# Optimization experiments

Measured on AMD Instinct MI355X. Metric: run time of the kernel, lower is better.

## Reference

```python
import jax, jax.numpy as jnp
import numpy as np

D_MODEL = 2048
N_HEADS = 16
D_HEAD = D_MODEL // N_HEADS  # 128
RANK = 32


def _orthogonal(key, rows, cols, dtype=jnp.float32):
    # mimic torch orthogonal init via QR
    a = jax.random.normal(key, (max(rows, cols), min(rows, cols)), dtype=jnp.float32)
    q, r = jnp.linalg.qr(a)
    q = q * jnp.sign(jnp.diagonal(r))
    if rows < cols:
        q = q.T
    return q.astype(dtype)


def setup_inputs() -> dict:
    key = jax.random.key(0)
    ks = jax.random.split(key, 8)
    B, T = 2, 2048
    x = jax.random.normal(ks[0], (B, T, D_MODEL), dtype=jnp.float32)
    s = 1.0 / np.sqrt(D_MODEL)
    Wq = jax.random.uniform(ks[1], (D_MODEL, D_MODEL), minval=-s, maxval=s, dtype=jnp.float32)
    Wk = jax.random.uniform(ks[2], (D_MODEL, D_MODEL), minval=-s, maxval=s, dtype=jnp.float32)
    Wv = jax.random.uniform(ks[3], (D_MODEL, D_MODEL), minval=-s, maxval=s, dtype=jnp.float32)
    Wo = jax.random.uniform(ks[4], (D_MODEL, D_MODEL), minval=-s, maxval=s, dtype=jnp.float32)
    # vein projector: project d_head -> rank, reconstruct rank -> d_head (orthogonal init)
    Wdown = _orthogonal(ks[5], D_HEAD, RANK)   # [d_head, r]
    Wup = _orthogonal(ks[6], RANK, D_HEAD)     # [r, d_head]
    return {"x": x, "Wq": Wq, "Wk": Wk, "Wv": Wv, "Wo": Wo, "Wdown": Wdown, "Wup": Wup}


def reference(x, Wq, Wk, Wv, Wo, Wdown, Wup):
    B, T, D = x.shape
    H, dh, r = N_HEADS, D_HEAD, RANK
    scale = 1.0 / np.sqrt(r)

    def heads(y):  # [B,T,D] -> [B,H,T,dh]
        return y.reshape(B, T, H, dh).transpose(0, 2, 1, 3)

    q = heads(x @ Wq.T)
    k = heads(x @ Wk.T)
    v = heads(x @ Wv.T)

    # project into vein (rank) space: [B,H,T,r]
    q_r = jnp.einsum('bhtd,dr->bhtr', q, Wdown)
    k_r = jnp.einsum('bhtd,dr->bhtr', k, Wdown)
    v_r = jnp.einsum('bhtd,dr->bhtr', v, Wdown)

    scores = jnp.einsum('bhqr,bhkr->bhqk', q_r, k_r) * scale  # [B,H,T,T]
    attn = jax.nn.softmax(scores, axis=-1)
    y_r = jnp.einsum('bhqk,bhkr->bhqr', attn, v_r)            # [B,H,T,r]
    y = jnp.einsum('bhtr,rd->bhtd', y_r, Wup)                  # reconstruct [B,H,T,dh]
    y = y.transpose(0, 2, 1, 3).reshape(B, T, D)
    out = y @ Wo.T
    return out
```

## Files before the change

### kernel.cpp

```cpp
#include <hip/hip_runtime.h>
#include <cstdint>
#include <cstddef>

typedef __bf16 bf16;
typedef __attribute__((ext_vector_type(8))) __bf16 bf16x8;
typedef __attribute__((ext_vector_type(4))) __bf16 bf16x4;
typedef __attribute__((ext_vector_type(2))) __bf16 bf16x2;
typedef __attribute__((ext_vector_type(4))) float f32x4;
typedef unsigned int u32;

#define D_MODEL 2048
#define QSCALE      0.17677669529663687f
#define QSCALE_L2E  (0.17677669529663687f * 1.4426950408889634f)

__device__ inline void async_load16(const void* gp, void* lp) {
  __builtin_amdgcn_global_load_lds(
      (const __attribute__((address_space(1))) u32*)gp,
      (__attribute__((address_space(3))) u32*)lp, 16, 0, 0);
}

__device__ inline float fast_exp2(float x) {
#if __has_builtin(__builtin_amdgcn_exp2f)
  return __builtin_amdgcn_exp2f(x);
#else
  return __expf(x * 0.6931471805599453f);
#endif
}

__global__ __launch_bounds__(256) void prep_k(
    const float* __restrict__ x,  const float* __restrict__ Wq,
    const float* __restrict__ Wk, const float* __restrict__ Wv,
    const float* __restrict__ Wo, const float* __restrict__ Wdown,
    const float* __restrict__ Wup,
    bf16* __restrict__ xb, bf16* __restrict__ EffT,
    bf16* __restrict__ WoEffT) {
  __shared__ __align__(16) char smem_[40960];
  const int bid = blockIdx.x;
  const int t = threadIdx.x;

  if (bid < 768) {
    const int mh = bid % 48;
    const int dblk = bid / 48;
    const float* W = (mh < 16) ? Wq : ((mh < 32) ? Wk : Wv);
    const int hrow = (mh & 15) * 128;
    const int d = dblk * 128 + (t & 127);
    const int rh = (t >> 7) * 16;
    const int rhs = __builtin_amdgcn_readfirstlane(rh);
    const float* wdn = Wdown + rhs;
    float acc[16];
#pragma unroll
    for (int j = 0; j < 16; ++j) acc[j] = 0.f;
    for (int kb = 0; kb < 16; ++kb) {
      float wv[8];
#pragma unroll
      for (int u = 0; u < 8; ++u)
        wv[u] = W[(size_t)(hrow + kb * 8 + u) * D_MODEL + d];
#pragma unroll
      for (int u = 0; u < 8; ++u) {
#pragma unroll
        for (int j = 0; j < 16; ++j)
          acc[j] += wv[u] * wdn[(kb * 8 + u) * 32 + j];
      }
    }
    bf16* outp = EffT + (size_t)(mh * 32 + rh) * D_MODEL + d;
#pragma unroll
    for (int j = 0; j < 16; ++j) outp[(size_t)j * D_MODEL] = (bf16)acc[j];
    return;
  }

  if (bid >= 1024) {
    const int tid = (bid - 1024) * 256 + t;
    float4 v[8];
#pragma unroll
    for (int p = 0; p < 4; ++p) {
      const int i = (tid + p * 262144) * 8;
      v[2 * p]     = *(const float4*)(x + i);
      v[2 * p + 1] = *(const float4*)(x + i + 4);
    }
#pragma unroll
    for (int p = 0; p < 4; ++p) {
      const int i = (tid + p * 262144) * 8;
      bf16x8 o;
      o[0] = (bf16)v[2*p].x;   o[1] = (bf16)v[2*p].y;
      o[2] = (bf16)v[2*p].z;   o[3] = (bf16)v[2*p].w;
      o[4] = (bf16)v[2*p+1].x; o[5] = (bf16)v[2*p+1].y;
      o[6] = (bf16)v[2*p+1].z; o[7] = (bf16)v[2*p+1].w;
      *(bf16x8*)(xb + i) = o;
    }
    return;
  }

  bf16* As_ = (bf16*)smem_;
  bf16* Bs_ = (bf16*)(smem_ + 32768);
  const int rel = bid - 768;
  const int d0 = (rel & 15) * 128, h = rel >> 4;
  const int wave = t >> 6, lane = t & 63;
  const int quad = lane >> 4, lc = lane & 15;
#pragma unroll
  for (int a = 0; a < 8; ++a) {
    int cc = a * 256 + t;
    int row = cc >> 4, c = cc & 15;
    const float* src = Wo + (size_t)(d0 + row) * 2048 + h * 128 + c * 8;
    float4 f0 = ((const float4*)src)[0], f1 = ((const float4*)src)[1];
    bf16x8 v;
    v[0] = (bf16)f0.x; v[1] = (bf16)f0.y; v[2] = (bf16)f0.z; v[3] = (bf16)f0.w;
    v[4] = (bf16)f1.x; v[5] = (bf16)f1.y; v[6] = (bf16)f1.z; v[7] = (bf16)f1.w;
    *(bf16x8*)(As_ + row * 128 + ((c ^ (row & 15)) * 8)) = v;
  }
  {
    int row = t >> 3;
    int c0 = (t & 7) * 2;
    const float* src = Wup + row * 128 + c0 * 8;
    float4 f0 = ((const float4*)src)[0], f1 = ((const float4*)src)[1];
    float4 f2 = ((const float4*)src)[2], f3 = ((const float4*)src)[3];
    bf16x8 b0, b1;
    b0[0] = (bf16)f0.x; b0[1] = (bf16)f0.y; b0[2] = (bf16)f0.z; b0[3] = (bf16)f0.w;
    b0[4] = (bf16)f1.x; b0[5] = (bf16)f1.y; b0[6] = (bf16)f1.z; b0[7] = (bf16)f1.w;
    b1[0] = (bf16)f2.x; b1[1] = (bf16)f2.y; b1[2] = (bf16)f2.z; b1[3] = (bf16)f2.w;
    b1[4] = (bf16)f3.x; b1[5] = (bf16)f3.y; b1[6] = (bf16)f3.z; b1[7] = (bf16)f3.w;
    *(bf16x8*)(Bs_ + row * 128 + ((c0 ^ (row & 15)) * 8)) = b0;
    *(bf16x8*)(Bs_ + row * 128 + (((c0 + 1) ^ (row & 15)) * 8)) = b1;
  }
  __syncthreads();
  f32x4 acc[2][2] = {};
  const int wm = wave * 32;
#pragma unroll
  for (int kc = 0; kc < 4; ++kc) {
    bf16x8 af[2], bfr[2];
#pragma unroll
    for (int mi = 0; mi < 2; ++mi) {
      int m = wm + mi * 16 + lc;
      af[mi] = *(const bf16x8*)(As_ + m * 128 + (((kc * 4 + quad) ^ (m & 15)) * 8));
    }
#pragma unroll
    for (int ni = 0; ni < 2; ++ni) {
      int n = ni * 16 + lc;
      bfr[ni] = *(const bf16x8*)(Bs_ + n * 128 + (((kc * 4 + quad) ^ (n & 15)) * 8));
    }
#pragma unroll
    for (int mi = 0; mi < 2; ++mi)
#pragma unroll
      for (int ni = 0; ni < 2; ++ni)
        acc[mi][ni] = __builtin_amdgcn_mfma_f32_16x16x32_bf16(
            af[mi], bfr[ni], acc[mi][ni], 0, 0, 0);
  }
#pragma unroll
  for (int mi = 0; mi < 2; ++mi)
#pragma unroll
    for (int ni = 0; ni < 2; ++ni)
#pragma unroll
      for (int reg = 0; reg < 4; ++reg)
        WoEffT[(size_t)(d0 + wm + mi * 16 + quad * 4 + reg) * 512 + h * 32 +
               ni * 16 + lc] = (bf16)acc[mi][ni][reg];
}

template <int EPI, int BM>
__global__ __launch_bounds__(256, (BM == 64 ? 3 : 2)) void gemm_bt_k(
    const bf16* __restrict__ A, const bf16* __restrict__ Bt,
    void* __restrict__ Cv, int M, int N, int K) {
  constexpr int MI = BM / 32;
  constexpr int AR = BM / 4;
  __shared__ __align__(16) bf16 As[2][BM * 64];
  __shared__ __align__(16) bf16 Bs[2][128 * 64];
  const int t = threadIdx.x, wave = t >> 6, lane = t & 63;
  const int quad = lane >> 4, lc = lane & 15;
  const size_t m0 = (size_t)blockIdx.x * BM;
  const size_t n0 = (size_t)blockIdx.y * 128;
  const int wm = (wave >> 1) * (MI * 16), wn = (wave & 1) * 64;
  const int sr = lane >> 3, ss = lane & 7;
  const bf16* Aga[MI]; const bf16* Bga[4]; int LoffA[MI], LoffB[4];
#pragma unroll
  for (int a = 0; a < MI; ++a) {
    int row = wave * AR + a * 8 + sr;
    Aga[a] = A + (m0 + row) * (size_t)K + (ss ^ (row & 7)) * 8;
    LoffA[a] = (wave * AR + a * 8) * 64;
  }
#pragma unroll
  for (int a = 0; a < 4; ++a) {
    int row = wave * 32 + a * 8 + sr;
    Bga[a] = Bt + (n0 + row) * (size_t)K + (ss ^ (row & 7)) * 8;
    LoffB[a] = (wave * 32 + a * 8) * 64;
  }
  f32x4 acc[MI][4] = {};
  const int NIT = K >> 6;
#pragma unroll
  for (int a = 0; a < MI; ++a) async_load16(Aga[a], &As[0][LoffA[a]]);
#pragma unroll
  for (int a = 0; a < 4; ++a) async_load16(Bga[a], &Bs[0][LoffB[a]]);
  __syncthreads();
  for (int it = 0; it < NIT; ++it) {
    const int cur = it & 1;
    if (it + 1 < NIT) {
      const int k0 = (it + 1) * 64;
#pragma unroll
      for (int a = 0; a < MI; ++a) async_load16(Aga[a] + k0, &As[1 - cur][LoffA[a]]);
#pragma unroll
      for (int a = 0; a < 4; ++a) async_load16(Bga[a] + k0, &Bs[1 - cur][LoffB[a]]);
    }
    const bf16* Asb = As[cur];
    const bf16* Bsb = Bs[cur];
#pragma unroll
    for (int kc = 0; kc < 2; ++kc) {
      bf16x8 af[MI], bfr[4];
#pragma unroll
      for (int mi = 0; mi < MI; ++mi) {
        int m = wm + mi * 16 + lc;
        af[mi] = *(const bf16x8*)(Asb + m * 64 + (((kc * 4 + quad) ^ (m & 7)) * 8));
      }
#pragma unroll
      for (int ni = 0; ni < 4; ++ni) {
        int n = wn + ni * 16 + lc;
        bfr[ni] = *(const bf16x8*)(Bsb + n * 64 + (((kc * 4 + quad) ^ (n & 7)) * 8));
      }
#pragma unroll
      for (int mi = 0; mi < MI; ++mi)
#pragma unroll
        for (int ni = 0; ni < 4; ++ni)
          acc[mi][ni] = __builtin_amdgcn_mfma_f32_16x16x32_bf16(
              af[mi], bfr[ni], acc[mi][ni], 0, 0, 0);
    }
    __syncthreads();
  }

  if (EPI == 0) {
    float* C = (float*)Cv;
#pragma unroll
    for (int mi = 0; mi < MI; ++mi)
#pragma unroll
      for (int ni = 0; ni < 4; ++ni) {
        size_t row = m0 + wm + mi * 16 + quad * 4;
        size_t col = n0 + wn + ni * 16 + lc;
#pragma unroll
        for (int reg = 0; reg < 4; ++reg)
          C[(row + reg) * (size_t)N + col] = acc[mi][ni][reg];
      }
  } else {
    bf16* C = (bf16*)Cv;
#pragma unroll
    for (int mi = 0; mi < MI; ++mi)
#pragma unroll
      for (int ni = 0; ni < 4; ++ni) {
        int n = (int)n0 + wn + ni * 16 + lc;
        int mat = n >> 9, hh = (n >> 5) & 15, r = n & 31;
        float sc = (mat == 0) ? QSCALE_L2E : 1.0f;
        int trow = (int)m0 + wm + mi * 16 + quad * 4;
        int b = trow >> 11, tl = trow & 2047;
        if (mat == 2) {
          int tile = tl >> 7, kin = tl & 127;
          size_t off = ((size_t)(b * 16 + hh) * 3 + 2) * 65536 +
                       (size_t)tile * 4096 + r * 128 +
                       (((kin >> 3) ^ (r & 15)) << 3) + (kin & 7);
          bf16x4 pk;
#pragma unroll
          for (int reg = 0; reg < 4; ++reg) pk[reg] = (bf16)acc[mi][ni][reg];
          *(bf16x4*)(C + off) = pk;
        } else {
#pragma unroll
          for (int reg = 0; reg < 4; ++reg) {
            size_t off = (((size_t)(b * 16 + hh) * 3 + mat) * 2048 + tl + reg) * 32 + r;
            C[off] = (bf16)(acc[mi][ni][reg] * sc);
          }
        }
      }
  }
}

__global__ __launch_bounds__(256, 4) void attn_k(const bf16* __restrict__ QKVr,
                                                 float* __restrict__ Op,
                                                 float* __restrict__ Sums) {
  const int bh = blockIdx.x, qb = blockIdx.y, kvh = blockIdx.z;
  const size_t base = (size_t)bh * 3 * 65536;
  const bf16* Q   = QKVr + base;
  const bf16* Kr  = Q + 65536 + (size_t)kvh * 1024 * 32;
  const bf16* Vrb = Q + 131072 + (size_t)kvh * 8 * 4096;
  __shared__ __align__(16) bf16 Ks[2][128 * 32];
  __shared__ __align__(16) bf16 Vt[2][32 * 128];
  __shared__ __align__(16) bf16 Ps[4 * 32 * 32];
  const int t = threadIdx.x, wave = t >> 6, lane = t & 63;
  const int quad = lane >> 4, lc = lane & 15;
  const int qbase = qb * 128 + wave * 32;
  const bf16x8 qf0 = *(const bf16x8*)(Q + (size_t)(qbase + lc) * 32 + quad * 8);
  const bf16x8 qf1 = *(const bf16x8*)(Q + (size_t)(qbase + 16 + lc) * 32 + quad * 8);
  f32x4 o00 = {}, o01 = {}, o10 = {}, o11 = {};
  f32x4 os0 = {}, os1 = {};
  bf16x8 ones;
#pragma unroll
  for (int j = 0; j < 8; ++j) ones[j] = (bf16)1.0f;
  const int krow = wave * 16 + (lane >> 2);
  const bf16* Kg = Kr + (size_t)krow * 32 + ((lane & 3) ^ ((krow >> 1) & 3)) * 8;
  bf16* pw = Ps + wave * 32 * 32;
  const int psw = (lc & 3) ^ (lc >> 2);

  async_load16(Kg, &Ks[0][wave * 16 * 32]);
  async_load16(Kg + (size_t)64 * 32, &Ks[0][(64 + wave * 16) * 32]);
  async_load16(Vrb + (wave * 2) * 512 + lane * 8, &Vt[0][(wave * 2) * 512]);
  async_load16(Vrb + (wave * 2 + 1) * 512 + lane * 8, &Vt[0][(wave * 2 + 1) * 512]);
  __syncthreads();

  for (int it = 0; it < 8; ++it) {
    const int kt = it * 128, cur = it & 1;
    if (it < 7) {
      async_load16(Kg + (size_t)(kt + 128) * 32, &Ks[1 - cur][wave * 16 * 32]);
      async_load16(Kg + (size_t)(kt + 192) * 32, &Ks[1 - cur][(64 + wave * 16) * 32]);
      const bf16* vg = Vrb + (size_t)(it + 1) * 4096;
      async_load16(vg + (wave * 2) * 512 + lane * 8, &Vt[1 - cur][(wave * 2) * 512]);
      async_load16(vg + (wave * 2 + 1) * 512 + lane * 8, &Vt[1 - cur][(wave * 2 + 1) * 512]);
    }
    const bf16* ksb = Ks[cur];
    const bf16* vtb = Vt[cur];
#pragma unroll
    for (int qtr = 0; qtr < 4; ++qtr) {
#pragma unroll
      for (int nii = 0; nii < 2; ++nii) {
        int ni = qtr * 2 + nii;
        int n = ni * 16 + lc;
        bf16x8 kf = *(const bf16x8*)(ksb + n * 32 + ((quad ^ ((n >> 1) & 3)) * 8));
        f32x4 z = {0.f, 0.f, 0.f, 0.f};
        f32x4 s0 = __builtin_amdgcn_mfma_f32_16x16x32_bf16(kf, qf0, z, 0, 0, 0);
        f32x4 s1 = __builtin_amdgcn_mfma_f32_16x16x32_bf16(kf, qf1, z, 0, 0, 0);
        bf16x4 p0, p1;
#pragma unroll
        for (int reg = 0; reg < 4; ++reg) {
          p0[reg] = (bf16)fast_exp2(s0[reg]);
          p1[reg] = (bf16)fast_exp2(s1[reg]);
        }
        int off = (((2 * nii + (quad >> 1)) ^ psw) * 8) + (quad & 1) * 4;
        *(bf16x4*)(pw + lc * 32 + off) = p0;
        *(bf16x4*)(pw + (16 + lc) * 32 + off) = p1;
      }
      int co = (quad ^ psw) * 8;
      bf16x8 pf0 = *(const bf16x8*)(pw + lc * 32 + co);
      bf16x8 pf1 = *(const bf16x8*)(pw + (16 + lc) * 32 + co);
      int vo = ((qtr * 4 + quad) ^ lc) * 8;
      bf16x8 v0 = *(const bf16x8*)(vtb + lc * 128 + vo);
      bf16x8 v1 = *(const bf16x8*)(vtb + (16 + lc) * 128 + vo);
      o00 = __builtin_amdgcn_mfma_f32_16x16x32_bf16(pf0, v0, o00, 0, 0, 0);
      o01 = __builtin_amdgcn_mfma_f32_16x16x32_bf16(pf0, v1, o01, 0, 0, 0);
      o10 = __builtin_amdgcn_mfma_f32_16x16x32_bf16(pf1, v0, o10, 0, 0, 0);
      o11 = __builtin_amdgcn_mfma_f32_16x16x32_bf16(pf1, v1, o11, 0, 0, 0);
      os0 = __builtin_amdgcn_mfma_f32_16x16x32_bf16(pf0, ones, os0, 0, 0, 0);
      os1 = __builtin_amdgcn_mfma_f32_16x16x32_bf16(pf1, ones, os1, 0, 0, 0);
    }
    __syncthreads();
  }
  const int b = bh >> 4, h = bh & 15;
  float* op = Op + (size_t)kvh * 4096 * 512;
#pragma unroll
  for (int reg = 0; reg < 4; ++reg) {
    size_t r0 = (size_t)b * 2048 + qbase + quad * 4 + reg;
    size_t r1 = r0 + 16;
    op[r0 * 512 + h * 32 + lc]      = o00[reg];
    op[r0 * 512 + h * 32 + 16 + lc] = o01[reg];
    op[r1 * 512 + h * 32 + lc]      = o10[reg];
    op[r1 * 512 + h * 32 + 16 + lc] = o11[reg];
  }
  if (lc == 0) {
    float* sp = Sums + (size_t)kvh * 65536 + (size_t)bh * 2048 + qbase;
#pragma unroll
    for (int reg = 0; reg < 4; ++reg) {
      sp[quad * 4 + reg]      = os0[reg];
      sp[16 + quad * 4 + reg] = os1[reg];
    }
  }
}

__global__ __launch_bounds__(256) void comb_k(const float* __restrict__ Op,
                                              const float* __restrict__ Sums,
                                              bf16* __restrict__ Yr) {
  const int idx = blockIdx.x * 256 + threadIdx.x;
  const int row = idx >> 6;
  const int c8 = (idx & 63) * 8;
  const int b = row >> 11, tl = row & 2047;
  const int h = c8 >> 5;
  const size_t si = (size_t)(b * 16 + h) * 2048 + tl;
  const float inv = 1.0f / (Sums[si] + Sums[65536 + si]);
  const float4* p0 = (const float4*)(Op + (size_t)row * 512 + c8);
  const float4* p1 = (const float4*)(Op + 4096 * 512 + (size_t)row * 512 + c8);
  float4 a0 = p0[0], a1 = p0[1];
  float4 b0 = p1[0], b1 = p1[1];
  bf16x8 o;
  o[0] = (bf16)((a0.x + b0.x) * inv); o[1] = (bf16)((a0.y + b0.y) * inv);
  o[2] = (bf16)((a0.z + b0.z) * inv); o[3] = (bf16)((a0.w + b0.w) * inv);
  o[4] = (bf16)((a1.x + b1.x) * inv); o[5] = (bf16)((a1.y + b1.y) * inv);
  o[6] = (bf16)((a1.z + b1.z) * inv); o[7] = (bf16)((a1.w + b1.w) * inv);
  *(bf16x8*)(Yr + (size_t)row * 512 + c8) = o;
}

extern "C" void kernel_launch(void* const* d_in, const int* in_sizes, int n_in,
                              void* d_out, int out_size, void* d_ws, size_t ws_size,
                              hipStream_t stream) {
  const float* x     = (const float*)d_in[0];
  const float* Wq    = (const float*)d_in[1];
  const float* Wk    = (const float*)d_in[2];
  const float* Wv    = (const float*)d_in[3];
  const float* Wo    = (const float*)d_in[4];
  const float* Wdown = (const float*)d_in[5];
  const float* Wup   = (const float*)d_in[6];
  float* out = (float*)d_out;

  char* ws = (char*)d_ws;
  bf16*  EffT   = (bf16*)(ws);
  float* Sums   = (float*)(ws);
  bf16*  WoEffT = (bf16*)(ws + 6291456);
  bf16*  QKVr   = (bf16*)(ws + 8388608);
  bf16*  Yrb    = (bf16*)(ws + 20971520);
  bf16*  xb     = (bf16*)(ws + 25165824);
  float* Opart  = (float*)(ws + 25165824);

  prep_k<<<dim3(2048), dim3(256), 0, stream>>>(x, Wq, Wk, Wv, Wo, Wdown, Wup,
                                               xb, EffT, WoEffT);
  gemm_bt_k<1, 64><<<dim3(64, 12), dim3(256), 0, stream>>>(xb, EffT, QKVr,
                                                           4096, 1536, 2048);
  attn_k<<<dim3(32, 16, 2), dim3(256), 0, stream>>>(QKVr, Opart, Sums);
  comb_k<<<dim3(1024), dim3(256), 0, stream>>>(Opart, Sums, Yrb);
  gemm_bt_k<0, 128><<<dim3(32, 16), dim3(256), 0, stream>>>(Yrb, WoEffT, out,
                                                            4096, 2048, 512);
}
```

Measured before the change: 224.4 us.

## Fuse fp32-to-bf16 conversion of x into QKV projection GEMM A-tile loads

The separate pass that converted x to bf16 inside prep_k is removed. The QKV GEMM now reads fp32 x directly, converts it in registers and writes swizzled bf16 tiles to shared memory, overlapping the next tile's global loads with the MFMA work. This removes one full write and read of the bf16 activation copy. The Wo-effective prep blocks are also re-split into smaller 64-row tiles so the prep grid shrinks, and the templated GEMM is split into two specialised kernels. The trade-off is that the A path moves from asynchronous direct-to-LDS loads to register-staged loads, which raises register pressure and doubles the bytes read for A inside the GEMM.

```diff
diff --git a/kernel.cpp b/kernel.cpp
--- a/kernel.cpp
+++ b/kernel.cpp
@@ -27,14 +27,19 @@
 #endif
 }
 
+__device__ inline bf16x8 cvt8(float4 a, float4 b) {
+  bf16x8 o;
+  o[0] = (bf16)a.x; o[1] = (bf16)a.y; o[2] = (bf16)a.z; o[3] = (bf16)a.w;
+  o[4] = (bf16)b.x; o[5] = (bf16)b.y; o[6] = (bf16)b.z; o[7] = (bf16)b.w;
+  return o;
+}
+
 __global__ __launch_bounds__(256) void prep_k(
-    const float* __restrict__ x,  const float* __restrict__ Wq,
-    const float* __restrict__ Wk, const float* __restrict__ Wv,
-    const float* __restrict__ Wo, const float* __restrict__ Wdown,
-    const float* __restrict__ Wup,
-    bf16* __restrict__ xb, bf16* __restrict__ EffT,
-    bf16* __restrict__ WoEffT) {
-  __shared__ __align__(16) char smem_[40960];
+    const float* __restrict__ Wq, const float* __restrict__ Wk,
+    const float* __restrict__ Wv, const float* __restrict__ Wo,
+    const float* __restrict__ Wdown, const float* __restrict__ Wup,
+    bf16* __restrict__ EffT, bf16* __restrict__ WoEffT) {
+  __shared__ __align__(16) char smem_[24576];
   const int bid = blockIdx.x;
   const int t = threadIdx.x;
 
@@ -68,44 +73,19 @@
     return;
   }
 
-  if (bid >= 1024) {
-    const int tid = (bid - 1024) * 256 + t;
-    float4 v[8];
-#pragma unroll
-    for (int p = 0; p < 4; ++p) {
-      const int i = (tid + p * 262144) * 8;
-      v[2 * p]     = *(const float4*)(x + i);
-      v[2 * p + 1] = *(const float4*)(x + i + 4);
-    }
-#pragma unroll
-    for (int p = 0; p < 4; ++p) {
-      const int i = (tid + p * 262144) * 8;
-      bf16x8 o;
-      o[0] = (bf16)v[2*p].x;   o[1] = (bf16)v[2*p].y;
-      o[2] = (bf16)v[2*p].z;   o[3] = (bf16)v[2*p].w;
-      o[4] = (bf16)v[2*p+1].x; o[5] = (bf16)v[2*p+1].y;
-      o[6] = (bf16)v[2*p+1].z; o[7] = (bf16)v[2*p+1].w;
-      *(bf16x8*)(xb + i) = o;
-    }
-    return;
-  }
-
   bf16* As_ = (bf16*)smem_;
-  bf16* Bs_ = (bf16*)(smem_ + 32768);
+  bf16* Bs_ = (bf16*)(smem_ + 16384);
   const int rel = bid - 768;
-  const int d0 = (rel & 15) * 128, h = rel >> 4;
+  const int d0 = (rel & 31) * 64, h = rel >> 5;
   const int wave = t >> 6, lane = t & 63;
   const int quad = lane >> 4, lc = lane & 15;
 #pragma unroll
-  for (int a = 0; a < 8; ++a) {
+  for (int a = 0; a < 4; ++a) {
     int cc = a * 256 + t;
     int row = cc >> 4, c = cc & 15;
     const float* src = Wo + (size_t)(d0 + row) * 2048 + h * 128 + c * 8;
     float4 f0 = ((const float4*)src)[0], f1 = ((const float4*)src)[1];
-    bf16x8 v;
-    v[0] = (bf16)f0.x; v[1] = (bf16)f0.y; v[2] = (bf16)f0.z; v[3] = (bf16)f0.w;
-    v[4] = (bf16)f1.x; v[5] = (bf16)f1.y; v[6] = (bf16)f1.z; v[7] = (bf16)f1.w;
-    *(bf16x8*)(As_ + row * 128 + ((c ^ (row & 15)) * 8)) = v;
+    *(bf16x8*)(As_ + row * 128 + ((c ^ (row & 15)) * 8)) = cvt8(f0, f1);
   }
   {
     int row = t >> 3;
@@ -113,97 +93,183 @@
     const float* src = Wup + row * 128 + c0 * 8;
     float4 f0 = ((const float4*)src)[0], f1 = ((const float4*)src)[1];
     float4 f2 = ((const float4*)src)[2], f3 = ((const float4*)src)[3];
-    bf16x8 b0, b1;
-    b0[0] = (bf16)f0.x; b0[1] = (bf16)f0.y; b0[2] = (bf16)f0.z; b0[3] = (bf16)f0.w;
-    b0[4] = (bf16)f1.x; b0[5] = (bf16)f1.y; b0[6] = (bf16)f1.z; b0[7] = (bf16)f1.w;
-    b1[0] = (bf16)f2.x; b1[1] = (bf16)f2.y; b1[2] = (bf16)f2.z; b1[3] = (bf16)f2.w;
-    b1[4] = (bf16)f3.x; b1[5] = (bf16)f3.y; b1[6] = (bf16)f3.z; b1[7] = (bf16)f3.w;
-    *(bf16x8*)(Bs_ + row * 128 + ((c0 ^ (row & 15)) * 8)) = b0;
-    *(bf16x8*)(Bs_ + row * 128 + (((c0 + 1) ^ (row & 15)) * 8)) = b1;
+    *(bf16x8*)(Bs_ + row * 128 + ((c0 ^ (row & 15)) * 8)) = cvt8(f0, f1);
+    *(bf16x8*)(Bs_ + row * 128 + (((c0 + 1) ^ (row & 15)) * 8)) = cvt8(f2, f3);
   }
   __syncthreads();
-  f32x4 acc[2][2] = {};
-  const int wm = wave * 32;
+  f32x4 acc[2] = {};
+  const int wm = wave * 16;
 #pragma unroll
   for (int kc = 0; kc < 4; ++kc) {
-    bf16x8 af[2], bfr[2];
-#pragma unroll
-    for (int mi = 0; mi < 2; ++mi) {
-      int m = wm + mi * 16 + lc;
-      af[mi] = *(const bf16x8*)(As_ + m * 128 + (((kc * 4 + quad) ^ (m & 15)) * 8));
-    }
+    int m = wm + lc;
+    bf16x8 af = *(const bf16x8*)(As_ + m * 128 + (((kc * 4 + quad) ^ (m & 15)) * 8));
 #pragma unroll
     for (int ni = 0; ni < 2; ++ni) {
       int n = ni * 16 + lc;
-      bfr[ni] = *(const bf16x8*)(Bs_ + n * 128 + (((kc * 4 + quad) ^ (n & 15)) * 8));
-    }
-#pragma unroll
-    for (int mi = 0; mi < 2; ++mi)
-#pragma unroll
-      for (int ni = 0; ni < 2; ++ni)
-        acc[mi][ni] = __builtin_amdgcn_mfma_f32_16x16x32_bf16(
-            af[mi], bfr[ni], acc[mi][ni], 0, 0, 0);
-  }
-#pragma unroll
-  for (int mi = 0; mi < 2; ++mi)
-#pragma unroll
-    for (int ni = 0; ni < 2; ++ni)
-#pragma unroll
-      for (int reg = 0; reg < 4; ++reg)
-        WoEffT[(size_t)(d0 + wm + mi * 16 + quad * 4 + reg) * 512 + h * 32 +
-               ni * 16 + lc] = (bf16)acc[mi][ni][reg];
-}
-
-template <int EPI, int BM>
-__global__ __launch_bounds__(256, (BM == 64 ? 3 : 2)) void gemm_bt_k(
-    const bf16* __restrict__ A, const bf16* __restrict__ Bt,
-    void* __restrict__ Cv, int M, int N, int K) {
-  constexpr int MI = BM / 32;
-  constexpr int AR = BM / 4;
-  __shared__ __align__(16) bf16 As[2][BM * 64];
+      bf16x8 bfr = *(const bf16x8*)(Bs_ + n * 128 + (((kc * 4 + quad) ^ (n & 15)) * 8));
+      acc[ni] = __builtin_amdgcn_mfma_f32_16x16x32_bf16(af, bfr, acc[ni], 0, 0, 0);
+    }
+  }
+#pragma unroll
+  for (int ni = 0; ni < 2; ++ni)
+#pragma unroll
+    for (int reg = 0; reg < 4; ++reg)
+      WoEffT[(size_t)(d0 + wm + quad * 4 + reg) * 512 + h * 32 +
+             ni * 16 + lc] = (bf16)acc[ni][reg];
+}
+
+__global__ __launch_bounds__(256, 3) void gemm1_k(
+    const float* __restrict__ Ax, const bf16* __restrict__ Bt,
+    bf16* __restrict__ C, int M, int N, int K) {
+  __shared__ __align__(16) bf16 As[2][64 * 64];
   __shared__ __align__(16) bf16 Bs[2][128 * 64];
   const int t = threadIdx.x, wave = t >> 6, lane = t & 63;
   const int quad = lane >> 4, lc = lane & 15;
-  const size_t m0 = (size_t)blockIdx.x * BM;
+  const size_t m0 = (size_t)blockIdx.x * 64;
   const size_t n0 = (size_t)blockIdx.y * 128;
-  const int wm = (wave >> 1) * (MI * 16), wn = (wave & 1) * 64;
+  const int wm = (wave >> 1) * 32, wn = (wave & 1) * 64;
   const int sr = lane >> 3, ss = lane & 7;
-  const bf16* Aga[MI]; const bf16* Bga[4]; int LoffA[MI], LoffB[4];
-#pragma unroll
-  for (int a = 0; a < MI; ++a) {
-    int row = wave * AR + a * 8 + sr;
-    Aga[a] = A + (m0 + row) * (size_t)K + (ss ^ (row & 7)) * 8;
-    LoffA[a] = (wave * AR + a * 8) * 64;
-  }
+  const int arow = t >> 2;
+  const int ac0 = (t & 3) * 2;
+  const float* Aga = Ax + (m0 + arow) * (size_t)K + ac0 * 8;
+  bf16* aw0;
+  bf16* aw1;
+  {
+    int s0 = (ac0 ^ (arow & 7)) * 8, s1 = ((ac0 + 1) ^ (arow & 7)) * 8;
+    aw0 = (bf16*)As + arow * 64 + s0;
+    aw1 = (bf16*)As + arow * 64 + s1;
+  }
+  const bf16* Bga[4]; int LoffB[4];
 #pragma unroll
   for (int a = 0; a < 4; ++a) {
     int row = wave * 32 + a * 8 + sr;
     Bga[a] = Bt + (n0 + row) * (size_t)K + (ss ^ (row & 7)) * 8;
     LoffB[a] = (wave * 32 + a * 8) * 64;
   }
-  f32x4 acc[MI][4] = {};
+  f32x4 acc[2][4] = {};
   const int NIT = K >> 6;
-#pragma unroll
-  for (int a = 0; a < MI; ++a) async_load16(Aga[a], &As[0][LoffA[a]]);
+  {
+    float4 a0 = ((const float4*)Aga)[0], a1 = ((const float4*)Aga)[1];
+    float4 a2 = ((const float4*)Aga)[2], a3 = ((const float4*)Aga)[3];
+    *(bf16x8*)aw0 = cvt8(a0, a1);
+    *(bf16x8*)aw1 = cvt8(a2, a3);
+  }
 #pragma unroll
   for (int a = 0; a < 4; ++a) async_load16(Bga[a], &Bs[0][LoffB[a]]);
+  __syncthreads();
+  for (int it = 0; it < NIT; ++it) {
+    const int cur = it & 1;
+    float4 a0, a1, a2, a3;
+    if (it + 1 < NIT) {
+      const int k0 = (it + 1) * 64;
+      const float* src = Aga + k0;
+      a0 = ((const float4*)src)[0]; a1 = ((const float4*)src)[1];
+      a2 = ((const float4*)src)[2]; a3 = ((const float4*)src)[3];
+#pragma unroll
+      for (int a = 0; a < 4; ++a) async_load16(Bga[a] + k0, &Bs[1 - cur][LoffB[a]]);
+    }
+    const bf16* Asb = As[cur];
+    const bf16* Bsb = Bs[cur];
+#pragma unroll
+    for (int kc = 0; kc < 2; ++kc) {
+      bf16x8 af[2], bfr[4];
+#pragma unroll
+      for (int mi = 0; mi < 2; ++mi) {
+        int m = wm + mi * 16 + lc;
+        af[mi] = *(const bf16x8*)(Asb + m * 64 + (((kc * 4 + quad) ^ (m & 7)) * 8));
+      }
+#pragma unroll
+      for (int ni = 0; ni < 4; ++ni) {
+        int n = wn + ni * 16 + lc;
+        bfr[ni] = *(const bf16x8*)(Bsb + n * 64 + (((kc * 4 + quad) ^ (n & 7)) * 8));
+      }
+#pragma unroll
+      for (int mi = 0; mi < 2; ++mi)
+#pragma unroll
+        for (int ni = 0; ni < 4; ++ni)
+          acc[mi][ni] = __builtin_amdgcn_mfma_f32_16x16x32_bf16(
+              af[mi], bfr[ni], acc[mi][ni], 0, 0, 0);
+    }
+    if (it + 1 < NIT) {
+      bf16* w0 = aw0 + (1 - cur) * 4096;
+      bf16* w1 = aw1 + (1 - cur) * 4096;
+      *(bf16x8*)w0 = cvt8(a0, a1);
+      *(bf16x8*)w1 = cvt8(a2, a3);
+    }
+    __syncthreads();
+  }
+#pragma unroll
+  for (int mi = 0; mi < 2; ++mi)
+#pragma unroll
+    for (int ni = 0; ni < 4; ++ni) {
+      int n = (int)n0 + wn + ni * 16 + lc;
+      int mat = n >> 9, hh = (n >> 5) & 15, r = n & 31;
+      float sc = (mat == 0) ? QSCALE_L2E : 1.0f;
+      int trow = (int)m0 + wm + mi * 16 + quad * 4;
+      int b = trow >> 11, tl = trow & 2047;
+      if (mat == 2) {
+        int tile = tl >> 7, kin = tl & 127;
+        size_t off = ((size_t)(b * 16 + hh) * 3 + 2) * 65536 +
+                     (size_t)tile * 4096 + r * 128 +
+                     (((kin >> 3) ^ (r & 15)) << 3) + (kin & 7);
+        bf16x4 pk;
+#pragma unroll
+        for (int reg = 0; reg < 4; ++reg) pk[reg] = (bf16)acc[mi][ni][reg];
+        *(bf16x4*)(C + off) = pk;
+      } else {
+#pragma unroll
+        for (int reg = 0; reg < 4; ++reg) {
+          size_t off = (((size_t)(b * 16 + hh) * 3 + mat) * 2048 + tl + reg) * 32 + r;
+          C[off] = (bf16)(acc[mi][ni][reg] * sc);
+        }
+      }
+    }
+}
+
+__global__ __launch_bounds__(256, 2) void gemm0_k(
+    const bf16* __restrict__ A, const bf16* __restrict__ Bt,
+    float* __restrict__ C, int M, int N, int K) {
+  __shared__ __align__(16) bf16 As[2][128 * 64];
+  __shared__ __align__(16) bf16 Bs[2][128 * 64];
+  const int t = threadIdx.x, wave = t >> 6, lane = t & 63;
+  const int quad = lane >> 4, lc = lane & 15;
+  const size_t m0 = (size_t)blockIdx.x * 128;
+  const size_t n0 = (size_t)blockIdx.y * 128;
+  const int wm = (wave >> 1) * 64, wn = (wave & 1) * 64;
+  const int sr = lane >> 3, ss = lane & 7;
+  const bf16* Aga[4]; const bf16* Bga[4]; int Loff[4];
+#pragma unroll
+  for (int a = 0; a < 4; ++a) {
+    int row = wave * 32 + a * 8 + sr;
+    Aga[a] = A + (m0 + row) * (size_t)K + (ss ^ (row & 7)) * 8;
+    Bga[a] = Bt + (n0 + row) * (size_t)K + (ss ^ (row & 7)) * 8;
+    Loff[a] = (wave * 32 + a * 8) * 64;
+  }
+  f32x4 acc[4][4] = {};
+  const int NIT = K >> 6;
+#pragma unroll
+  for (int a = 0; a < 4; ++a) {
+    async_load16(Aga[a], &As[0][Loff[a]]);
+    async_load16(Bga[a], &Bs[0][Loff[a]]);
+  }
   __syncthreads();
   for (int it = 0; it < NIT; ++it) {
     const int cur = it & 1;
     if (it + 1 < NIT) {
       const int k0 = (it + 1) * 64;
 #pragma unroll
-      for (int a = 0; a < MI; ++a) async_load16(Aga[a] + k0, &As[1 - cur][LoffA[a]]);
-#pragma unroll
-      for (int a = 0; a < 4; ++a) async_load16(Bga[a] + k0, &Bs[1 - cur][LoffB[a]]);
+      for (int a = 0; a < 4; ++a) {
+        async_load16(Aga[a] + k0, &As[1 - cur][Loff[a]]);
+        async_load16(Bga[a] + k0, &Bs[1 - cur][Loff[a]]);
+      }
     }
     const bf16* Asb = As[cur];
     const bf16* Bsb = Bs[cur];
 #pragma unroll
     for (int kc = 0; kc < 2; ++kc) {
-      bf16x8 af[MI], bfr[4];
-#pragma unroll
-      for (int mi = 0; mi < MI; ++mi) {
+      bf16x8 af[4], bfr[4];
+#pragma unroll
+      for (int mi = 0; mi < 4; ++mi) {
         int m = wm + mi * 16 + lc;
         af[mi] = *(const bf16x8*)(Asb + m * 64 + (((kc * 4 + quad) ^ (m & 7)) * 8));
       }
@@ -213,7 +279,7 @@
         bfr[ni] = *(const bf16x8*)(Bsb + n * 64 + (((kc * 4 + quad) ^ (n & 7)) * 8));
       }
 #pragma unroll
-      for (int mi = 0; mi < MI; ++mi)
+      for (int mi = 0; mi < 4; ++mi)
 #pragma unroll
         for (int ni = 0; ni < 4; ++ni)
           acc[mi][ni] = __builtin_amdgcn_mfma_f32_16x16x32_bf16(
@@ -221,48 +287,16 @@
     }
     __syncthreads();
   }
-
-  if (EPI == 0) {
-    float* C = (float*)Cv;
-#pragma unroll
-    for (int mi = 0; mi < MI; ++mi)
-#pragma unroll
-      for (int ni = 0; ni < 4; ++ni) {
-        size_t row = m0 + wm + mi * 16 + quad * 4;
-        size_t col = n0 + wn + ni * 16 + lc;
-#pragma unroll
-        for (int reg = 0; reg < 4; ++reg)
-          C[(row + reg) * (size_t)N + col] = acc[mi][ni][reg];
-      }
-  } else {
-    bf16* C = (bf16*)Cv;
-#pragma unroll
-    for (int mi = 0; mi < MI; ++mi)
-#pragma unroll
-      for (int ni = 0; ni < 4; ++ni) {
-        int n = (int)n0 + wn + ni * 16 + lc;
-        int mat = n >> 9, hh = (n >> 5) & 15, r = n & 31;
-        float sc = (mat == 0) ? QSCALE_L2E : 1.0f;
-        int trow = (int)m0 + wm + mi * 16 + quad * 4;
-        int b = trow >> 11, tl = trow & 2047;
-        if (mat == 2) {
-          int tile = tl >> 7, kin = tl & 127;
-          size_t off = ((size_t)(b * 16 + hh) * 3 + 2) * 65536 +
-                       (size_t)tile * 4096 + r * 128 +
-                       (((kin >> 3) ^ (r & 15)) << 3) + (kin & 7);
-          bf16x4 pk;
-#pragma unroll
-          for (int reg = 0; reg < 4; ++reg) pk[reg] = (bf16)acc[mi][ni][reg];
-          *(bf16x4*)(C + off) = pk;
-        } else {
-#pragma unroll
-          for (int reg = 0; reg < 4; ++reg) {
-            size_t off = (((size_t)(b * 16 + hh) * 3 + mat) * 2048 + tl + reg) * 32 + r;
-            C[off] = (bf16)(acc[mi][ni][reg] * sc);
-          }
-        }
-      }
-  }
+#pragma unroll
+  for (int mi = 0; mi < 4; ++mi)
+#pragma unroll
+    for (int ni = 0; ni < 4; ++ni) {
+      size_t row = m0 + wm + mi * 16 + quad * 4;
+      size_t col = n0 + wn + ni * 16 + lc;
+#pragma unroll
+      for (int reg = 0; reg < 4; ++reg)
+        C[(row + reg) * (size_t)N + col] = acc[mi][ni][reg];
+    }
 }
 
 __global__ __launch_bounds__(256, 4) void attn_k(const bf16* __restrict__ QKVr,
@@ -404,15 +438,14 @@
   bf16*  WoEffT = (bf16*)(ws + 6291456);
   bf16*  QKVr   = (bf16*)(ws + 8388608);
   bf16*  Yrb    = (bf16*)(ws + 20971520);
-  bf16*  xb     = (bf16*)(ws + 25165824);
   float* Opart  = (float*)(ws + 25165824);
 
-  prep_k<<<dim3(2048), dim3(256), 0, stream>>>(x, Wq, Wk, Wv, Wo, Wdown, Wup,
-                                               xb, EffT, WoEffT);
-  gemm_bt_k<1, 64><<<dim3(64, 12), dim3(256), 0, stream>>>(xb, EffT, QKVr,
-                                                           4096, 1536, 2048);
+  prep_k<<<dim3(1280), dim3(256), 0, stream>>>(Wq, Wk, Wv, Wo, Wdown, Wup,
+                                               EffT, WoEffT);
+  gemm1_k<<<dim3(64, 12), dim3(256), 0, stream>>>(x, EffT, QKVr,
+                                                  4096, 1536, 2048);
   attn_k<<<dim3(32, 16, 2), dim3(256), 0, stream>>>(QKVr, Opart, Sums);
   comb_k<<<dim3(1024), dim3(256), 0, stream>>>(Opart, Sums, Yrb);
-  gemm_bt_k<0, 128><<<dim3(32, 16), dim3(256), 0, stream>>>(Yrb, WoEffT, out,
-                                                            4096, 2048, 512);
-}
+  gemm0_k<<<dim3(32, 16), dim3(256), 0, stream>>>(Yrb, WoEffT, out,
+                                                  4096, 2048, 512);
+}
```

New measurement: 247.2 us. +10.2%, slower.
